# Kernel tuning notes

Hardware: AMD Instinct MI355X
Metric: run time of the kernel (lower is better)

The kernel has to match this reference:

```python
import jax, jax.numpy as jnp
import numpy as np

K_IN = 9      # input_patch_size
K_OUT = 3     # output_patch_size
C_IN = 4      # nb_of_input_features
C_OUT = 2     # nb_of_output_features
HID = 50      # int_layer_width
B, H, W = 16, 128, 128
CUT = K_IN // 2 - K_OUT // 2  # border pixels cut from output (3)


def _unfold(x, k):
    # x: [B, C, H, W] -> [B, C*k*k, L] with torch unfold ordering (c, ki, kj)
    b, c, h, w = x.shape
    ho, wo = h - k + 1, w - k + 1
    cols = jnp.stack([x[:, :, i:i + ho, j:j + wo]
                      for i in range(k) for j in range(k)], axis=2)  # [B,C,k*k,ho,wo]
    return cols.reshape(b, c * k * k, ho * wo)


def _fold_add(patches, oh, ow):
    # patches: [B, C, k, k, ho, wo] -> overlap-add into [B, C, oh, ow]
    b, c, k, _, ho, wo = patches.shape
    out = jnp.zeros((b, c, oh, ow), dtype=patches.dtype)
    for i in range(k):
        for j in range(k):
            out = out.at[:, :, i:i + ho, j:j + wo].add(patches[:, :, i, j])
    return out


def setup_inputs() -> dict:
    key = jax.random.key(0)
    ks = jax.random.split(key, 7)
    f_in = C_IN * K_IN * K_IN      # 324
    f_out = C_OUT * K_OUT * K_OUT  # 18
    s1 = 1.0 / np.sqrt(f_in)
    s2 = 1.0 / np.sqrt(HID)
    return {
        "x": jax.random.normal(ks[0], (B, C_IN, H, W), dtype=jnp.float32),
        "W1": jax.random.uniform(ks[1], (f_in, HID), jnp.float32, -s1, s1),
        "b1": jax.random.uniform(ks[2], (HID,), jnp.float32, -s1, s1),
        "W2": jax.random.uniform(ks[3], (HID, HID), jnp.float32, -s2, s2),
        "b2": jax.random.uniform(ks[4], (HID,), jnp.float32, -s2, s2),
        "W3": jax.random.uniform(ks[5], (HID, f_out), jnp.float32, -s2, s2),
        "b3": jax.random.uniform(ks[6], (f_out,), jnp.float32, -s2, s2),
    }


def reference(x, W1, b1, W2, b2, W3, b3):
    b, c, h, w = x.shape
    oh, ow = h - 2 * CUT, w - 2 * CUT          # 122, 122
    ho, wo = h - K_IN + 1, w - K_IN + 1        # 120, 120 (= oh-K_OUT+1)
    # unfold -> [B, L, C_in*K_in^2] -> flatten rows
    cols = _unfold(x, K_IN)                    # [B, 324, L]
    feats = cols.transpose(0, 2, 1).reshape(b * ho * wo, -1)
    # 3-layer MLP
    hmid = jax.nn.relu(feats @ W1 + b1)
    hmid = jax.nn.relu(hmid @ W2 + b2)
    out = hmid @ W3 + b3                       # [B*L, C_out*K_out^2]
    # fold (overlap-add), torch feature ordering (c, ki, kj)
    patches = out.reshape(b, ho, wo, C_OUT, K_OUT, K_OUT)
    patches = patches.transpose(0, 3, 4, 5, 1, 2)  # [B, C_out, k, k, ho, wo]
    res = _fold_add(patches, oh, ow)
    # divisor = fold(unfold(ones)) -> per-pixel overlap count
    ones_patches = jnp.ones((1, 1, K_OUT, K_OUT, ho, wo), dtype=x.dtype)
    divisor = _fold_add(ones_patches, oh, ow)  # [1,1,oh,ow]
    return res / divisor
```

## Files before the change

### kernel.cpp

```cpp
#include <hip/hip_runtime.h>
#include <hip/hip_bf16.h>

#define BATCH   16
#define C_INF   4
#define H_IN    128
#define W_IN    128
#define HID     50
#define F_OUT   18
#define HO      120
#define WO      120
#define OH      122
#define OW      122
#define NPOS    (BATCH * HO * WO)
#define MBLK    128
#define NBLKS   (NPOS / MBLK)

#define NB1     (11*4*2*64*8)
#define NB2     (2*4*2*64*8)
#define NB3     (2*2*2*64*8)
#define NWF     (NB1 + NB2 + NB3)
#define NXP     (BATCH*C_INF*H_IN*W_IN)
#define WOFF    (NPOS * F_OUT)

typedef float  v4f    __attribute__((ext_vector_type(4)));
typedef short  short8 __attribute__((ext_vector_type(8)));
typedef __bf16 v8bf   __attribute__((ext_vector_type(8)));
typedef int    v4i    __attribute__((ext_vector_type(4)));
typedef uint   u32x4  __attribute__((ext_vector_type(4)));
typedef u32x4  u32x4_a4 __attribute__((aligned(4)));

__device__ inline short f2bf_hi(float x) {
    __hip_bfloat16 h = __float2bfloat16(x);
    return __builtin_bit_cast(short, h);
}
__device__ inline float bf2f(short s) {
    __hip_bfloat16 h = __builtin_bit_cast(__hip_bfloat16, s);
    return __bfloat162float(h);
}
__device__ inline uint hipair(uint a, uint b) { return __builtin_amdgcn_perm(b, a, 0x07060302u); }

__device__ inline int slot_to_k1(int s, int qb, int e) {
    if (s < 9) {
        int pair = s*4 + qb;
        int c = pair/9, ki = pair - c*9;
        return c*81 + ki*9 + e;
    }
    int r = (s-9)*32 + qb*8 + e;
    if (r >= 36) return -1;
    int c = r/9, ki = r - c*9;
    return c*81 + ki*9 + 8;
}

__global__ __launch_bounds__(256)
void prep_kernel(const float* __restrict__ x,
                 const float* __restrict__ W1, const float* __restrict__ W2,
                 const float* __restrict__ W3,
                 uint* __restrict__ xp, short* __restrict__ wf)
{
    int i = blockIdx.x * 256 + threadIdx.x;
    if (i < NXP) {
        float v = x[i];
        short hi = f2bf_hi(v);
        short lo = f2bf_hi(v - bf2f(hi));
        xp[i] = ((uint)(ushort)hi << 16) | (uint)(ushort)lo;
        return;
    }
    i -= NXP;
    if (i >= NWF) return;
    float val;
    int p;
    if (i < NB1) {
        int t = i;
        int e = t & 7, lane = (t >> 3) & 63; p = (t >> 9) & 1;
        int rest = t >> 10;
        int u = rest & 3, s = rest >> 2;
        int k = slot_to_k1(s, lane >> 4, e);
        int n = u*16 + (lane & 15);
        val = (k >= 0 && n < HID) ? W1[k*HID + n] : 0.f;
    } else if (i < NB1 + NB2) {
        int t = i - NB1;
        int e = t & 7, lane = (t >> 3) & 63; p = (t >> 9) & 1;
        int rest = t >> 10;
        int u = rest & 3, s = rest >> 2;
        int k = s*32 + ((lane >> 4) << 3) + e;
        int n = u*16 + (lane & 15);
        val = (k < HID && n < HID) ? W2[k*HID + n] : 0.f;
    } else {
        int t = i - NB1 - NB2;
        int e = t & 7, lane = (t >> 3) & 63; p = (t >> 9) & 1;
        int rest = t >> 10;
        int u = rest & 1, s = rest >> 1;
        int k = s*32 + ((lane >> 4) << 3) + e;
        int n = u*16 + (lane & 15);
        val = (k < HID && n < F_OUT) ? W3[k*F_OUT + n] : 0.f;
    }
    short hi = f2bf_hi(val);
    wf[i] = (p == 0) ? hi : f2bf_hi(val - bf2f(hi));
}

__global__ __launch_bounds__(256, 4)
void mfma_mlp(const uint* __restrict__ xp,
              const float* __restrict__ b1, const float* __restrict__ b2,
              const float* __restrict__ b3,
              const short* __restrict__ wf, float* __restrict__ out3)
{
    __shared__ short h_hi[128 * 72];

    const int tid  = threadIdx.x;
    const int lane = tid & 63;
    const int w    = tid >> 6;
    const int q    = lane >> 4, col = lane & 15;
    const int mbase = blockIdx.x * MBLK;
    const int mw    = w * 32;

    float bias1[4], bias2[4], bias3[2];
    #pragma unroll
    for (int u = 0; u < 4; ++u) {
        int j = u*16 + col;
        bias1[u] = (j < HID) ? b1[j] : 0.f;
        bias2[u] = (j < HID) ? b2[j] : 0.f;
    }
    #pragma unroll
    for (int u = 0; u < 2; ++u) {
        int j = u*16 + col;
        bias3[u] = (j < F_OUT) ? b3[j] : 0.f;
    }

    int xbase[2];
    #pragma unroll
    for (int t = 0; t < 2; ++t) {
        int pos = mbase + mw + t*16 + col;
        int b   = pos / (HO*WO); int rem = pos - b*(HO*WO);
        int y   = rem / WO;      int xc  = rem - y*WO;
        xbase[t] = b*(C_INF*H_IN*W_IN) + y*W_IN + xc;
    }

    const v4i* B1 = (const v4i*)wf;
    const v4i* B2 = (const v4i*)(wf + NB1);
    const v4i* B3 = (const v4i*)(wf + NB1 + NB2);

    v4f acc[2][4];
    #pragma unroll
    for (int t = 0; t < 2; ++t)
        #pragma unroll
        for (int u = 0; u < 4; ++u)
            acc[t][u] = (v4f){0.f, 0.f, 0.f, 0.f};

    #pragma unroll 3
    for (int s = 0; s < 9; ++s) {
        const int pair = s*4 + q;
        const int c = pair/9, ki = pair - c*9;
        const int off = c*(H_IN*W_IN) + ki*W_IN;

        v4i bhv[4], blv[4];
        #pragma unroll
        for (int u = 0; u < 4; ++u) {
            int fb = ((s*4 + u)*2)*64 + lane;
            bhv[u] = B1[fb];
            blv[u] = B1[fb + 64];
        }

        u32x4 wa[2], wb[2];
        #pragma unroll
        for (int t = 0; t < 2; ++t) {
            const uint* p = &xp[xbase[t] + off];
            wa[t] = *(const u32x4_a4*)(p);
            wb[t] = *(const u32x4_a4*)(p + 4);
        }
        short8 ah[2];
        #pragma unroll
        for (int t = 0; t < 2; ++t) {
            u32x4 hh;
            hh.x = hipair(wa[t].x, wa[t].y); hh.y = hipair(wa[t].z, wa[t].w);
            hh.z = hipair(wb[t].x, wb[t].y); hh.w = hipair(wb[t].z, wb[t].w);
            ah[t] = __builtin_bit_cast(short8, hh);
        }
        #pragma unroll
        for (int u = 0; u < 4; ++u) {
            v8bf bh = __builtin_bit_cast(v8bf, bhv[u]);
            v8bf bl = __builtin_bit_cast(v8bf, blv[u]);
            #pragma unroll
            for (int t = 0; t < 2; ++t) {
                v8bf a_h = __builtin_bit_cast(v8bf, ah[t]);
                acc[t][u] = __builtin_amdgcn_mfma_f32_16x16x32_bf16(a_h, bh, acc[t][u], 0, 0, 0);
                acc[t][u] = __builtin_amdgcn_mfma_f32_16x16x32_bf16(a_h, bl, acc[t][u], 0, 0, 0);
            }
        }
    }
    #pragma unroll
    for (int sr = 0; sr < 2; ++sr) {
        const int s = 9 + sr;
        short8 ah[2];
        #pragma unroll
        for (int e = 0; e < 8; ++e) {
            int r = sr*32 + q*8 + e;
            bool valid = (r < 36);
            int c = valid ? r/9 : 0;
            int ki = r - c*9;
            int off = c*(H_IN*W_IN) + ki*W_IN + 8;
            #pragma unroll
            for (int t = 0; t < 2; ++t) {
                uint wv = valid ? xp[xbase[t] + off] : 0u;
                ah[t][e] = (short)(wv >> 16);
            }
        }
        #pragma unroll
        for (int u = 0; u < 4; ++u) {
            int fb = ((s*4 + u)*2)*64 + lane;
            v8bf bh = __builtin_bit_cast(v8bf, B1[fb]);
            v8bf bl = __builtin_bit_cast(v8bf, B1[fb + 64]);
            #pragma unroll
            for (int t = 0; t < 2; ++t) {
                v8bf a_h = __builtin_bit_cast(v8bf, ah[t]);
                acc[t][u] = __builtin_amdgcn_mfma_f32_16x16x32_bf16(a_h, bh, acc[t][u], 0, 0, 0);
                acc[t][u] = __builtin_amdgcn_mfma_f32_16x16x32_bf16(a_h, bl, acc[t][u], 0, 0, 0);
            }
        }
    }

    #pragma unroll
    for (int u = 0; u < 4; ++u) {
        #pragma unroll
        for (int t = 0; t < 2; ++t) {
            #pragma unroll
            for (int r = 0; r < 4; ++r) {
                float v = fmaxf(acc[t][u][r] + bias1[u], 0.f);
                int m = mw + t*16 + q*4 + r;
                h_hi[m*72 + u*16 + col] = f2bf_hi(v);
            }
        }
    }

    v4f acc2[2][4];
    #pragma unroll
    for (int t = 0; t < 2; ++t)
        #pragma unroll
        for (int u = 0; u < 4; ++u)
            acc2[t][u] = (v4f){0.f, 0.f, 0.f, 0.f};

    #pragma unroll
    for (int s = 0; s < 2; ++s) {
        short8 ah2[2];
        #pragma unroll
        for (int t = 0; t < 2; ++t) {
            int m = mw + t*16 + col;
            ah2[t] = *(const short8*)&h_hi[m*72 + s*32 + q*8];
        }
        #pragma unroll
        for (int u = 0; u < 4; ++u) {
            int fb = ((s*4 + u)*2)*64 + lane;
            v8bf bh = __builtin_bit_cast(v8bf, B2[fb]);
            v8bf bl = __builtin_bit_cast(v8bf, B2[fb + 64]);
            #pragma unroll
            for (int t = 0; t < 2; ++t) {
                v8bf a_h = __builtin_bit_cast(v8bf, ah2[t]);
                acc2[t][u] = __builtin_amdgcn_mfma_f32_16x16x32_bf16(a_h, bh, acc2[t][u], 0, 0, 0);
                acc2[t][u] = __builtin_amdgcn_mfma_f32_16x16x32_bf16(a_h, bl, acc2[t][u], 0, 0, 0);
            }
        }
    }

    #pragma unroll
    for (int u = 0; u < 4; ++u) {
        #pragma unroll
        for (int t = 0; t < 2; ++t) {
            #pragma unroll
            for (int r = 0; r < 4; ++r) {
                float v = fmaxf(acc2[t][u][r] + bias2[u], 0.f);
                int m = mw + t*16 + q*4 + r;
                h_hi[m*72 + u*16 + col] = f2bf_hi(v);
            }
        }
    }

    v4f acc3[2][2];
    #pragma unroll
    for (int t = 0; t < 2; ++t)
        #pragma unroll
        for (int u = 0; u < 2; ++u)
            acc3[t][u] = (v4f){0.f, 0.f, 0.f, 0.f};

    #pragma unroll
    for (int s = 0; s < 2; ++s) {
        short8 ah3[2];
        #pragma unroll
        for (int t = 0; t < 2; ++t) {
            int m = mw + t*16 + col;
            ah3[t] = *(const short8*)&h_hi[m*72 + s*32 + q*8];
        }
        #pragma unroll
        for (int u = 0; u < 2; ++u) {
            int fb = ((s*2 + u)*2)*64 + lane;
            v8bf bh = __builtin_bit_cast(v8bf, B3[fb]);
            v8bf bl = __builtin_bit_cast(v8bf, B3[fb + 64]);
            #pragma unroll
            for (int t = 0; t < 2; ++t) {
                v8bf a_h = __builtin_bit_cast(v8bf, ah3[t]);
                acc3[t][u] = __builtin_amdgcn_mfma_f32_16x16x32_bf16(a_h, bh, acc3[t][u], 0, 0, 0);
                acc3[t][u] = __builtin_amdgcn_mfma_f32_16x16x32_bf16(a_h, bl, acc3[t][u], 0, 0, 0);
            }
        }
    }

    #pragma unroll
    for (int u = 0; u < 2; ++u) {
        int j = u*16 + col;
        if (j < F_OUT) {
            #pragma unroll
            for (int t = 0; t < 2; ++t) {
                v4f vs;
                #pragma unroll
                for (int r = 0; r < 4; ++r) vs[r] = acc3[t][u][r] + bias3[u];
                *(v4f*)&out3[j*NPOS + mbase + mw + t*16 + q*4] = vs;
            }
        }
    }
}

__global__ __launch_bounds__(256)
void fold_kernel(const float* __restrict__ out3, float* __restrict__ out)
{
    const int idx = blockIdx.x * 256 + threadIdx.x;
    const int total = BATCH * 2 * OH * OW;
    if (idx >= total) return;

    int t = idx;
    const int ox = t % OW; t /= OW;
    const int oy = t % OH; t /= OH;
    const int c  = t & 1;  t >>= 1;
    const int b  = t;

    const int ylo = max(0, oy - 2), yhi = min(HO - 1, oy);
    const int xlo = max(0, ox - 2), xhi = min(WO - 1, ox);

    float s = 0.f;
    for (int y = ylo; y <= yhi; ++y) {
        const int ki = oy - y;
        for (int xx = xlo; xx <= xhi; ++xx) {
            const int kj = ox - xx;
            const int o  = (c*3 + ki)*3 + kj;
            s += out3[o*NPOS + (b*HO + y)*WO + xx];
        }
    }
    const float div = (float)((yhi - ylo + 1) * (xhi - xlo + 1));
    out[idx] = s / div;
}

extern "C" void kernel_launch(void* const* d_in, const int* in_sizes, int n_in,
                              void* d_out, int out_size, void* d_ws, size_t ws_size,
                              hipStream_t stream)
{
    const float* x  = (const float*)d_in[0];
    const float* W1 = (const float*)d_in[1];
    const float* b1 = (const float*)d_in[2];
    const float* W2 = (const float*)d_in[3];
    const float* b2 = (const float*)d_in[4];
    const float* W3 = (const float*)d_in[5];
    const float* b3 = (const float*)d_in[6];

    float* out3 = (float*)d_ws;
    short* wf   = (short*)(out3 + WOFF);
    uint*  xp   = (uint*)(wf + NWF);

    const int nprep = (NXP + NWF + 255) / 256;
    prep_kernel<<<nprep, 256, 0, stream>>>(x, W1, W2, W3, xp, wf);

    mfma_mlp<<<NBLKS, 256, 0, stream>>>(xp, b1, b2, b3, wf, out3);

    const int total = BATCH * 2 * OH * OW;
    fold_kernel<<<(total + 255) / 256, 256, 0, stream>>>(out3, (float*)d_out);
}
```

Baseline: 121.7 us.

## Fuse prep, MLP and fold into one persistent kernel with grid barriers

Merges the three kernel launches (weight/input bf16 split, MFMA MLP, overlap-add fold) into a single persistent kernel of 512 blocks that loops over work units. Stages are separated by atomic-counter grid barriers, and a memset clears the barrier counters on each call. The aim is to remove launch gaps and tail effects between stages. In exchange, occupancy drops to 2 blocks per CU with grid-stride loops, and the barrier relies on all 512 blocks being co-resident, with spin-wait overhead.

```diff
diff --git a/kernel.cpp b/kernel.cpp
--- a/kernel.cpp
+++ b/kernel.cpp
@@ -14,6 +14,8 @@
 #define NPOS    (BATCH * HO * WO)
 #define MBLK    128
 #define NBLKS   (NPOS / MBLK)
+#define NB      512
+#define NOUT    (BATCH * 2 * OH * OW)
 
 #define NB1     (11*4*2*64*8)
 #define NB2     (2*4*2*64*8)
@@ -51,67 +53,81 @@
     return c*81 + ki*9 + 8;
 }
 
-__global__ __launch_bounds__(256)
-void prep_kernel(const float* __restrict__ x,
-                 const float* __restrict__ W1, const float* __restrict__ W2,
-                 const float* __restrict__ W3,
-                 uint* __restrict__ xp, short* __restrict__ wf)
-{
-    int i = blockIdx.x * 256 + threadIdx.x;
-    if (i < NXP) {
-        float v = x[i];
-        short hi = f2bf_hi(v);
-        short lo = f2bf_hi(v - bf2f(hi));
-        xp[i] = ((uint)(ushort)hi << 16) | (uint)(ushort)lo;
-        return;
-    }
-    i -= NXP;
-    if (i >= NWF) return;
-    float val;
-    int p;
-    if (i < NB1) {
-        int t = i;
-        int e = t & 7, lane = (t >> 3) & 63; p = (t >> 9) & 1;
-        int rest = t >> 10;
-        int u = rest & 3, s = rest >> 2;
-        int k = slot_to_k1(s, lane >> 4, e);
-        int n = u*16 + (lane & 15);
-        val = (k >= 0 && n < HID) ? W1[k*HID + n] : 0.f;
-    } else if (i < NB1 + NB2) {
-        int t = i - NB1;
-        int e = t & 7, lane = (t >> 3) & 63; p = (t >> 9) & 1;
-        int rest = t >> 10;
-        int u = rest & 3, s = rest >> 2;
-        int k = s*32 + ((lane >> 4) << 3) + e;
-        int n = u*16 + (lane & 15);
-        val = (k < HID && n < HID) ? W2[k*HID + n] : 0.f;
-    } else {
-        int t = i - NB1 - NB2;
-        int e = t & 7, lane = (t >> 3) & 63; p = (t >> 9) & 1;
-        int rest = t >> 10;
-        int u = rest & 1, s = rest >> 1;
-        int k = s*32 + ((lane >> 4) << 3) + e;
-        int n = u*16 + (lane & 15);
-        val = (k < HID && n < F_OUT) ? W3[k*F_OUT + n] : 0.f;
-    }
-    short hi = f2bf_hi(val);
-    wf[i] = (p == 0) ? hi : f2bf_hi(val - bf2f(hi));
-}
-
-__global__ __launch_bounds__(256, 4)
-void mfma_mlp(const uint* __restrict__ xp,
-              const float* __restrict__ b1, const float* __restrict__ b2,
-              const float* __restrict__ b3,
-              const short* __restrict__ wf, float* __restrict__ out3)
+__device__ inline void gbar(uint* cnt, uint* flag) {
+    __syncthreads();
+    if (threadIdx.x == 0) {
+        __threadfence();
+        uint prev = __hip_atomic_fetch_add(cnt, 1u, __ATOMIC_ACQ_REL, __HIP_MEMORY_SCOPE_AGENT);
+        if (prev == NB - 1u) {
+            __hip_atomic_store(flag, 1u, __ATOMIC_RELEASE, __HIP_MEMORY_SCOPE_AGENT);
+        } else {
+            while (__hip_atomic_load(flag, __ATOMIC_ACQUIRE, __HIP_MEMORY_SCOPE_AGENT) == 0u)
+                __builtin_amdgcn_s_sleep(8);
+        }
+        __threadfence();
+    }
+    __syncthreads();
+}
+
+__global__ __launch_bounds__(256, 2)
+void fused_kernel(const float* __restrict__ x,
+                  const float* __restrict__ W1, const float* __restrict__ b1,
+                  const float* __restrict__ W2, const float* __restrict__ b2,
+                  const float* __restrict__ W3, const float* __restrict__ b3,
+                  uint* hdr,
+                  float* __restrict__ out3, short* __restrict__ wf,
+                  uint* __restrict__ xp, float* __restrict__ out)
 {
     __shared__ short h_hi[128 * 72];
 
     const int tid  = threadIdx.x;
+    const int bid  = blockIdx.x;
+
+    for (int gi = bid*256 + tid; gi < NXP + NWF; gi += NB*256) {
+        if (gi < NXP) {
+            float v = x[gi];
+            short hi = f2bf_hi(v);
+            short lo = f2bf_hi(v - bf2f(hi));
+            xp[gi] = ((uint)(ushort)hi << 16) | (uint)(ushort)lo;
+        } else {
+            int i = gi - NXP;
+            float val; int p;
+            if (i < NB1) {
+                int t = i;
+                int e = t & 7, lane = (t >> 3) & 63; p = (t >> 9) & 1;
+                int rest = t >> 10;
+                int u = rest & 3, s = rest >> 2;
+                int k = slot_to_k1(s, lane >> 4, e);
+                int n = u*16 + (lane & 15);
+                val = (k >= 0 && n < HID) ? W1[k*HID + n] : 0.f;
+            } else if (i < NB1 + NB2) {
+                int t = i - NB1;
+                int e = t & 7, lane = (t >> 3) & 63; p = (t >> 9) & 1;
+                int rest = t >> 10;
+                int u = rest & 3, s = rest >> 2;
+                int k = s*32 + ((lane >> 4) << 3) + e;
+                int n = u*16 + (lane & 15);
+                val = (k < HID && n < HID) ? W2[k*HID + n] : 0.f;
+            } else {
+                int t = i - NB1 - NB2;
+                int e = t & 7, lane = (t >> 3) & 63; p = (t >> 9) & 1;
+                int rest = t >> 10;
+                int u = rest & 1, s = rest >> 1;
+                int k = s*32 + ((lane >> 4) << 3) + e;
+                int n = u*16 + (lane & 15);
+                val = (k < HID && n < F_OUT) ? W3[k*F_OUT + n] : 0.f;
+            }
+            short hi = f2bf_hi(val);
+            wf[i] = (p == 0) ? hi : f2bf_hi(val - bf2f(hi));
+        }
+    }
+
+    gbar(&hdr[0], &hdr[1]);
+
     const int lane = tid & 63;
     const int w    = tid >> 6;
     const int q    = lane >> 4, col = lane & 15;
-    const int mbase = blockIdx.x * MBLK;
-    const int mw    = w * 32;
+    const int mw   = w * 32;
 
     float bias1[4], bias2[4], bias3[2];
     #pragma unroll
@@ -126,224 +142,224 @@
         bias3[u] = (j < F_OUT) ? b3[j] : 0.f;
     }
 
-    int xbase[2];
-    #pragma unroll
-    for (int t = 0; t < 2; ++t) {
-        int pos = mbase + mw + t*16 + col;
-        int b   = pos / (HO*WO); int rem = pos - b*(HO*WO);
-        int y   = rem / WO;      int xc  = rem - y*WO;
-        xbase[t] = b*(C_INF*H_IN*W_IN) + y*W_IN + xc;
-    }
-
     const v4i* B1 = (const v4i*)wf;
     const v4i* B2 = (const v4i*)(wf + NB1);
     const v4i* B3 = (const v4i*)(wf + NB1 + NB2);
 
-    v4f acc[2][4];
-    #pragma unroll
-    for (int t = 0; t < 2; ++t)
-        #pragma unroll
-        for (int u = 0; u < 4; ++u)
-            acc[t][u] = (v4f){0.f, 0.f, 0.f, 0.f};
-
-    #pragma unroll 3
-    for (int s = 0; s < 9; ++s) {
-        const int pair = s*4 + q;
-        const int c = pair/9, ki = pair - c*9;
-        const int off = c*(H_IN*W_IN) + ki*W_IN;
-
-        v4i bhv[4], blv[4];
+    for (int unit = bid; unit < NBLKS; unit += NB) {
+        const int mbase = unit * MBLK;
+
+        int xbase[2];
+        #pragma unroll
+        for (int t = 0; t < 2; ++t) {
+            int pos = mbase + mw + t*16 + col;
+            int b   = pos / (HO*WO); int rem = pos - b*(HO*WO);
+            int y   = rem / WO;      int xc  = rem - y*WO;
+            xbase[t] = b*(C_INF*H_IN*W_IN) + y*W_IN + xc;
+        }
+
+        v4f acc[2][4];
+        #pragma unroll
+        for (int t = 0; t < 2; ++t)
+            #pragma unroll
+            for (int u = 0; u < 4; ++u)
+                acc[t][u] = (v4f){0.f, 0.f, 0.f, 0.f};
+
+        #pragma unroll 3
+        for (int s = 0; s < 9; ++s) {
+            const int pair = s*4 + q;
+            const int c = pair/9, ki = pair - c*9;
+            const int off = c*(H_IN*W_IN) + ki*W_IN;
+
+            v4i bhv[4], blv[4];
+            #pragma unroll
+            for (int u = 0; u < 4; ++u) {
+                int fb = ((s*4 + u)*2)*64 + lane;
+                bhv[u] = B1[fb];
+                blv[u] = B1[fb + 64];
+            }
+
+            u32x4 wa[2], wb[2];
+            #pragma unroll
+            for (int t = 0; t < 2; ++t) {
+                const uint* p = &xp[xbase[t] + off];
+                wa[t] = *(const u32x4_a4*)(p);
+                wb[t] = *(const u32x4_a4*)(p + 4);
+            }
+            short8 ah[2];
+            #pragma unroll
+            for (int t = 0; t < 2; ++t) {
+                u32x4 hh;
+                hh.x = hipair(wa[t].x, wa[t].y); hh.y = hipair(wa[t].z, wa[t].w);
+                hh.z = hipair(wb[t].x, wb[t].y); hh.w = hipair(wb[t].z, wb[t].w);
+                ah[t] = __builtin_bit_cast(short8, hh);
+            }
+            #pragma unroll
+            for (int u = 0; u < 4; ++u) {
+                v8bf bh = __builtin_bit_cast(v8bf, bhv[u]);
+                v8bf bl = __builtin_bit_cast(v8bf, blv[u]);
+                #pragma unroll
+                for (int t = 0; t < 2; ++t) {
+                    v8bf a_h = __builtin_bit_cast(v8bf, ah[t]);
+                    acc[t][u] = __builtin_amdgcn_mfma_f32_16x16x32_bf16(a_h, bh, acc[t][u], 0, 0, 0);
+                    acc[t][u] = __builtin_amdgcn_mfma_f32_16x16x32_bf16(a_h, bl, acc[t][u], 0, 0, 0);
+                }
+            }
+        }
+        #pragma unroll
+        for (int sr = 0; sr < 2; ++sr) {
+            const int s = 9 + sr;
+            short8 ah[2];
+            #pragma unroll
+            for (int e = 0; e < 8; ++e) {
+                int r = sr*32 + q*8 + e;
+                bool valid = (r < 36);
+                int c = valid ? r/9 : 0;
+                int ki = r - c*9;
+                int off = c*(H_IN*W_IN) + ki*W_IN + 8;
+                #pragma unroll
+                for (int t = 0; t < 2; ++t) {
+                    uint wv = valid ? xp[xbase[t] + off] : 0u;
+                    ah[t][e] = (short)(wv >> 16);
+                }
+            }
+            #pragma unroll
+            for (int u = 0; u < 4; ++u) {
+                int fb = ((s*4 + u)*2)*64 + lane;
+                v8bf bh = __builtin_bit_cast(v8bf, B1[fb]);
+                v8bf bl = __builtin_bit_cast(v8bf, B1[fb + 64]);
+                #pragma unroll
+                for (int t = 0; t < 2; ++t) {
+                    v8bf a_h = __builtin_bit_cast(v8bf, ah[t]);
+                    acc[t][u] = __builtin_amdgcn_mfma_f32_16x16x32_bf16(a_h, bh, acc[t][u], 0, 0, 0);
+                    acc[t][u] = __builtin_amdgcn_mfma_f32_16x16x32_bf16(a_h, bl, acc[t][u], 0, 0, 0);
+                }
+            }
+        }
+
         #pragma unroll
         for (int u = 0; u < 4; ++u) {
-            int fb = ((s*4 + u)*2)*64 + lane;
-            bhv[u] = B1[fb];
-            blv[u] = B1[fb + 64];
-        }
-
-        u32x4 wa[2], wb[2];
-        #pragma unroll
-        for (int t = 0; t < 2; ++t) {
-            const uint* p = &xp[xbase[t] + off];
-            wa[t] = *(const u32x4_a4*)(p);
-            wb[t] = *(const u32x4_a4*)(p + 4);
-        }
-        short8 ah[2];
-        #pragma unroll
-        for (int t = 0; t < 2; ++t) {
-            u32x4 hh;
-            hh.x = hipair(wa[t].x, wa[t].y); hh.y = hipair(wa[t].z, wa[t].w);
-            hh.z = hipair(wb[t].x, wb[t].y); hh.w = hipair(wb[t].z, wb[t].w);
-            ah[t] = __builtin_bit_cast(short8, hh);
-        }
+            #pragma unroll
+            for (int t = 0; t < 2; ++t) {
+                #pragma unroll
+                for (int r = 0; r < 4; ++r) {
+                    float v = fmaxf(acc[t][u][r] + bias1[u], 0.f);
+                    int m = mw + t*16 + q*4 + r;
+                    h_hi[m*72 + u*16 + col] = f2bf_hi(v);
+                }
+            }
+        }
+
+        v4f acc2[2][4];
+        #pragma unroll
+        for (int t = 0; t < 2; ++t)
+            #pragma unroll
+            for (int u = 0; u < 4; ++u)
+                acc2[t][u] = (v4f){0.f, 0.f, 0.f, 0.f};
+
+        #pragma unroll
+        for (int s = 0; s < 2; ++s) {
+            short8 ah2[2];
+            #pragma unroll
+            for (int t = 0; t < 2; ++t) {
+                int m = mw + t*16 + col;
+                ah2[t] = *(const short8*)&h_hi[m*72 + s*32 + q*8];
+            }
+            #pragma unroll
+            for (int u = 0; u < 4; ++u) {
+                int fb = ((s*4 + u)*2)*64 + lane;
+                v8bf bh = __builtin_bit_cast(v8bf, B2[fb]);
+                v8bf bl = __builtin_bit_cast(v8bf, B2[fb + 64]);
+                #pragma unroll
+                for (int t = 0; t < 2; ++t) {
+                    v8bf a_h = __builtin_bit_cast(v8bf, ah2[t]);
+                    acc2[t][u] = __builtin_amdgcn_mfma_f32_16x16x32_bf16(a_h, bh, acc2[t][u], 0, 0, 0);
+                    acc2[t][u] = __builtin_amdgcn_mfma_f32_16x16x32_bf16(a_h, bl, acc2[t][u], 0, 0, 0);
+                }
+            }
+        }
+
         #pragma unroll
         for (int u = 0; u < 4; ++u) {
-            v8bf bh = __builtin_bit_cast(v8bf, bhv[u]);
-            v8bf bl = __builtin_bit_cast(v8bf, blv[u]);
-            #pragma unroll
-            for (int t = 0; t < 2; ++t) {
-                v8bf a_h = __builtin_bit_cast(v8bf, ah[t]);
-                acc[t][u] = __builtin_amdgcn_mfma_f32_16x16x32_bf16(a_h, bh, acc[t][u], 0, 0, 0);
-                acc[t][u] = __builtin_amdgcn_mfma_f32_16x16x32_bf16(a_h, bl, acc[t][u], 0, 0, 0);
-            }
-        }
-    }
-    #pragma unroll
-    for (int sr = 0; sr < 2; ++sr) {
-        const int s = 9 + sr;
-        short8 ah[2];
-        #pragma unroll
-        for (int e = 0; e < 8; ++e) {
-            int r = sr*32 + q*8 + e;
-            bool valid = (r < 36);
-            int c = valid ? r/9 : 0;
-            int ki = r - c*9;
-            int off = c*(H_IN*W_IN) + ki*W_IN + 8;
-            #pragma unroll
-            for (int t = 0; t < 2; ++t) {
-                uint wv = valid ? xp[xbase[t] + off] : 0u;
-                ah[t][e] = (short)(wv >> 16);
-            }
-        }
-        #pragma unroll
-        for (int u = 0; u < 4; ++u) {
-            int fb = ((s*4 + u)*2)*64 + lane;
-            v8bf bh = __builtin_bit_cast(v8bf, B1[fb]);
-            v8bf bl = __builtin_bit_cast(v8bf, B1[fb + 64]);
-            #pragma unroll
-            for (int t = 0; t < 2; ++t) {
-                v8bf a_h = __builtin_bit_cast(v8bf, ah[t]);
-                acc[t][u] = __builtin_amdgcn_mfma_f32_16x16x32_bf16(a_h, bh, acc[t][u], 0, 0, 0);
-                acc[t][u] = __builtin_amdgcn_mfma_f32_16x16x32_bf16(a_h, bl, acc[t][u], 0, 0, 0);
-            }
-        }
-    }
-
-    #pragma unroll
-    for (int u = 0; u < 4; ++u) {
-        #pragma unroll
-        for (int t = 0; t < 2; ++t) {
-            #pragma unroll
-            for (int r = 0; r < 4; ++r) {
-                float v = fmaxf(acc[t][u][r] + bias1[u], 0.f);
-                int m = mw + t*16 + q*4 + r;
-                h_hi[m*72 + u*16 + col] = f2bf_hi(v);
-            }
-        }
-    }
-
-    v4f acc2[2][4];
-    #pragma unroll
-    for (int t = 0; t < 2; ++t)
-        #pragma unroll
-        for (int u = 0; u < 4; ++u)
-            acc2[t][u] = (v4f){0.f, 0.f, 0.f, 0.f};
-
-    #pragma unroll
-    for (int s = 0; s < 2; ++s) {
-        short8 ah2[2];
-        #pragma unroll
-        for (int t = 0; t < 2; ++t) {
-            int m = mw + t*16 + col;
-            ah2[t] = *(const short8*)&h_hi[m*72 + s*32 + q*8];
-        }
-        #pragma unroll
-        for (int u = 0; u < 4; ++u) {
-            int fb = ((s*4 + u)*2)*64 + lane;
-            v8bf bh = __builtin_bit_cast(v8bf, B2[fb]);
-            v8bf bl = __builtin_bit_cast(v8bf, B2[fb + 64]);
-            #pragma unroll
-            for (int t = 0; t < 2; ++t) {
-                v8bf a_h = __builtin_bit_cast(v8bf, ah2[t]);
-                acc2[t][u] = __builtin_amdgcn_mfma_f32_16x16x32_bf16(a_h, bh, acc2[t][u], 0, 0, 0);
-                acc2[t][u] = __builtin_amdgcn_mfma_f32_16x16x32_bf16(a_h, bl, acc2[t][u], 0, 0, 0);
-            }
-        }
-    }
-
-    #pragma unroll
-    for (int u = 0; u < 4; ++u) {
-        #pragma unroll
-        for (int t = 0; t < 2; ++t) {
-            #pragma unroll
-            for (int r = 0; r < 4; ++r) {
-                float v = fmaxf(acc2[t][u][r] + bias2[u], 0.f);
-                int m = mw + t*16 + q*4 + r;
-                h_hi[m*72 + u*16 + col] = f2bf_hi(v);
-            }
-        }
-    }
-
-    v4f acc3[2][2];
-    #pragma unroll
-    for (int t = 0; t < 2; ++t)
-        #pragma unroll
-        for (int u = 0; u < 2; ++u)
-            acc3[t][u] = (v4f){0.f, 0.f, 0.f, 0.f};
-
-    #pragma unroll
-    for (int s = 0; s < 2; ++s) {
-        short8 ah3[2];
-        #pragma unroll
-        for (int t = 0; t < 2; ++t) {
-            int m = mw + t*16 + col;
-            ah3[t] = *(const short8*)&h_hi[m*72 + s*32 + q*8];
-        }
+            #pragma unroll
+            for (int t = 0; t < 2; ++t) {
+                #pragma unroll
+                for (int r = 0; r < 4; ++r) {
+                    float v = fmaxf(acc2[t][u][r] + bias2[u], 0.f);
+                    int m = mw + t*16 + q*4 + r;
+                    h_hi[m*72 + u*16 + col] = f2bf_hi(v);
+                }
+            }
+        }
+
+        v4f acc3[2][2];
+        #pragma unroll
+        for (int t = 0; t < 2; ++t)
+            #pragma unroll
+            for (int u = 0; u < 2; ++u)
+                acc3[t][u] = (v4f){0.f, 0.f, 0.f, 0.f};
+
+        #pragma unroll
+        for (int s = 0; s < 2; ++s) {
+            short8 ah3[2];
+            #pragma unroll
+            for (int t = 0; t < 2; ++t) {
+                int m = mw + t*16 + col;
+                ah3[t] = *(const short8*)&h_hi[m*72 + s*32 + q*8];
+            }
+            #pragma unroll
+            for (int u = 0; u < 2; ++u) {
+                int fb = ((s*2 + u)*2)*64 + lane;
+                v8bf bh = __builtin_bit_cast(v8bf, B3[fb]);
+                v8bf bl = __builtin_bit_cast(v8bf, B3[fb + 64]);
+                #pragma unroll
+                for (int t = 0; t < 2; ++t) {
+                    v8bf a_h = __builtin_bit_cast(v8bf, ah3[t]);
+                    acc3[t][u] = __builtin_amdgcn_mfma_f32_16x16x32_bf16(a_h, bh, acc3[t][u], 0, 0, 0);
+                    acc3[t][u] = __builtin_amdgcn_mfma_f32_16x16x32_bf16(a_h, bl, acc3[t][u], 0, 0, 0);
+                }
+            }
+        }
+
         #pragma unroll
         for (int u = 0; u < 2; ++u) {
-            int fb = ((s*2 + u)*2)*64 + lane;
-            v8bf bh = __builtin_bit_cast(v8bf, B3[fb]);
-            v8bf bl = __builtin_bit_cast(v8bf, B3[fb + 64]);
-            #pragma unroll
-            for (int t = 0; t < 2; ++t) {
-                v8bf a_h = __builtin_bit_cast(v8bf, ah3[t]);
-                acc3[t][u] = __builtin_amdgcn_mfma_f32_16x16x32_bf16(a_h, bh, acc3[t][u], 0, 0, 0);
-                acc3[t][u] = __builtin_amdgcn_mfma_f32_16x16x32_bf16(a_h, bl, acc3[t][u], 0, 0, 0);
-            }
-        }
-    }
-
-    #pragma unroll
-    for (int u = 0; u < 2; ++u) {
-        int j = u*16 + col;
-        if (j < F_OUT) {
-            #pragma unroll
-            for (int t = 0; t < 2; ++t) {
-                v4f vs;
-                #pragma unroll
-                for (int r = 0; r < 4; ++r) vs[r] = acc3[t][u][r] + bias3[u];
-                *(v4f*)&out3[j*NPOS + mbase + mw + t*16 + q*4] = vs;
-            }
-        }
-    }
-}
-
-__global__ __launch_bounds__(256)
-void fold_kernel(const float* __restrict__ out3, float* __restrict__ out)
-{
-    const int idx = blockIdx.x * 256 + threadIdx.x;
-    const int total = BATCH * 2 * OH * OW;
-    if (idx >= total) return;
-
-    int t = idx;
-    const int ox = t % OW; t /= OW;
-    const int oy = t % OH; t /= OH;
-    const int c  = t & 1;  t >>= 1;
-    const int b  = t;
-
-    const int ylo = max(0, oy - 2), yhi = min(HO - 1, oy);
-    const int xlo = max(0, ox - 2), xhi = min(WO - 1, ox);
-
-    float s = 0.f;
-    for (int y = ylo; y <= yhi; ++y) {
-        const int ki = oy - y;
-        for (int xx = xlo; xx <= xhi; ++xx) {
-            const int kj = ox - xx;
-            const int o  = (c*3 + ki)*3 + kj;
-            s += out3[o*NPOS + (b*HO + y)*WO + xx];
-        }
-    }
-    const float div = (float)((yhi - ylo + 1) * (xhi - xlo + 1));
-    out[idx] = s / div;
+            int j = u*16 + col;
+            if (j < F_OUT) {
+                #pragma unroll
+                for (int t = 0; t < 2; ++t) {
+                    v4f vs;
+                    #pragma unroll
+                    for (int r = 0; r < 4; ++r) vs[r] = acc3[t][u][r] + bias3[u];
+                    *(v4f*)&out3[j*NPOS + mbase + mw + t*16 + q*4] = vs;
+                }
+            }
+        }
+    }
+
+    gbar(&hdr[2], &hdr[3]);
+
+    for (int idx = bid*256 + tid; idx < NOUT; idx += NB*256) {
+        int t = idx;
+        const int ox = t % OW; t /= OW;
+        const int oy = t % OH; t /= OH;
+        const int c  = t & 1;  t >>= 1;
+        const int b  = t;
+
+        const int ylo = max(0, oy - 2), yhi = min(HO - 1, oy);
+        const int xlo = max(0, ox - 2), xhi = min(WO - 1, ox);
+
+        float s = 0.f;
+        for (int y = ylo; y <= yhi; ++y) {
+            const int ki = oy - y;
+            for (int xx = xlo; xx <= xhi; ++xx) {
+                const int kj = ox - xx;
+                const int o  = (c*3 + ki)*3 + kj;
+                s += out3[o*NPOS + (b*HO + y)*WO + xx];
+            }
+        }
+        const float div = (float)((yhi - ylo + 1) * (xhi - xlo + 1));
+        out[idx] = s / div;
+    }
 }
 
 extern "C" void kernel_launch(void* const* d_in, const int* in_sizes, int n_in,
@@ -358,15 +374,13 @@
     const float* W3 = (const float*)d_in[5];
     const float* b3 = (const float*)d_in[6];
 
-    float* out3 = (float*)d_ws;
+    uint*  hdr  = (uint*)d_ws;
+    float* out3 = (float*)d_ws + 4;
     short* wf   = (short*)(out3 + WOFF);
     uint*  xp   = (uint*)(wf + NWF);
 
-    const int nprep = (NXP + NWF + 255) / 256;
-    prep_kernel<<<nprep, 256, 0, stream>>>(x, W1, W2, W3, xp, wf);
-
-    mfma_mlp<<<NBLKS, 256, 0, stream>>>(xp, b1, b2, b3, wf, out3);
-
-    const int total = BATCH * 2 * OH * OW;
-    fold_kernel<<<(total + 255) / 256, 256, 0, stream>>>(out3, (float*)d_out);
-}
+    hipMemsetAsync(hdr, 0, 16, stream);
+
+    fused_kernel<<<NB, 256, 0, stream>>>(x, W1, b1, W2, b2, W3, b3,
+                                         hdr, out3, wf, xp, (float*)d_out);
+}
```

New measurement: 373.2 us. 207% more time.
